# Optimization experiments

Measured on AMD Instinct MI355X. Metric: run time of the kernel, lower is better.

Reference implementation:

```python
import jax, jax.numpy as jnp
import numpy as np

E, H, D = 1024, 16, 64
F = 4608          # max_ffn_size = int(1024*3*1.5)
BASE_FFN = 3072   # int(emb*3)
ADAPT = 0.5
CHUNK = 256


def rotate_half(x):
    x1 = x[..., ::2]
    x2 = x[..., 1::2]
    return jnp.stack((-x2, x1), axis=-1).reshape(x.shape[:-1] + (-1,))


def rms_norm(x, w, eps=1e-6):
    x = jnp.where(jnp.isnan(x) | jnp.isinf(x), jnp.zeros_like(x), x)
    rms = jnp.clip(jnp.sqrt(jnp.mean(x * x, axis=-1, keepdims=True) + eps), 1e-6, 1e6)
    return x / rms * w


def setup_inputs() -> dict:
    key = jax.random.key(0)
    ks = jax.random.split(key, 12)
    s = 0.02
    return {
        "x": jax.random.normal(ks[0], (2, 4096, E), dtype=jnp.float32),
        "w_qkv": jax.random.normal(ks[1], (E, 3 * E), dtype=jnp.float32) * s,
        "w_out": jax.random.normal(ks[2], (E, E), dtype=jnp.float32) * s,
        "g1": jnp.ones((E,), dtype=jnp.float32),
        "g2": jnp.ones((E,), dtype=jnp.float32),
        "w_dp1": jax.random.normal(ks[3], (E, E // 4), dtype=jnp.float32) * s,
        "w_dp2": jax.random.normal(ks[4], (E // 4, 1), dtype=jnp.float32) * s,
        "w_gate": jax.random.normal(ks[5], (E, F), dtype=jnp.float32) * s,
        "w_up": jax.random.normal(ks[6], (E, F), dtype=jnp.float32) * s,
        "w_down": jax.random.normal(ks[7], (F, E), dtype=jnp.float32) * s,
        "g_hidden": jnp.ones((F,), dtype=jnp.float32),
    }


def _linear_attention(x, w_qkv, w_out):
    B, L, _ = x.shape
    qkv = (x @ w_qkv).reshape(B, L, 3, H, D).transpose(2, 0, 3, 1, 4)  # [3,B,H,L,D]
    q, k, v = qkv[0], qkv[1], qkv[2]
    # RoPE (start_pos = 0)
    pos = jnp.arange(L, dtype=jnp.float32)
    inv_freq = 1.0 / (10000.0 ** (jnp.arange(0, D, 2, dtype=jnp.float32) / D))
    freqs = pos[:, None] * inv_freq[None, :]
    emb = jnp.concatenate([freqs, freqs], axis=-1)
    cos = jnp.cos(emb)[None, None]
    sin = jnp.sin(emb)[None, None]
    q = q * cos + rotate_half(q) * sin
    k = k * cos + rotate_half(k) * sin
    # elu + 1 feature map
    q = jax.nn.elu(q) + 1.0
    k = jax.nn.elu(k) + 1.0
    # chunk-wise cumulative recurrence (no cache path)
    NC = L // CHUNK
    def to_chunks(t):
        return jnp.moveaxis(t.reshape(B, H, NC, CHUNK, D), 2, 0)  # [NC,B,H,C,D]
    qc, kc, vc = to_chunks(q), to_chunks(k), to_chunks(v)

    def step(carry, inp):
        S, Z = carry  # S:[B,H,D,D], Z:[B,H,D]
        qi, ki, vi = inp
        kv = jnp.einsum('bhld,bhle->bhlde', ki, vi)
        kv_cum = jnp.cumsum(kv, axis=2) + S[:, :, None]
        k_cum = jnp.cumsum(ki, axis=2) + Z[:, :, None]
        num = jnp.einsum('bhld,bhlde->bhle', qi, kv_cum)
        den = jnp.einsum('bhld,bhld->bhl', qi, k_cum)
        return (kv_cum[:, :, -1], k_cum[:, :, -1]), (num, den)

    S0 = jnp.zeros((B, H, D, D), dtype=x.dtype)
    Z0 = jnp.zeros((B, H, D), dtype=x.dtype)
    _, (num, den) = jax.lax.scan(step, (S0, Z0), (qc, kc, vc))
    num = jnp.moveaxis(num, 0, 2).reshape(B, H, L, D)
    den = jnp.moveaxis(den, 0, 2).reshape(B, H, L)
    den = jnp.maximum(den, 1e-6)
    out = num / den[..., None]
    out = out.transpose(0, 2, 1, 3).reshape(B, L, H * D)
    return out @ w_out


def _adaptive_ffn(x, w_dp1, w_dp2, w_gate, w_up, w_down, g_hidden):
    x_mean = x.mean(axis=1)                                   # [B,E]
    dim_ratio = jax.nn.sigmoid(jax.nn.silu(x_mean @ w_dp1) @ w_dp2)  # [B,1]
    ratio = jnp.clip(1.0 + (dim_ratio - 0.5) * 2.0 * ADAPT, 1.0 - ADAPT, 1.0 + ADAPT)
    size = jnp.maximum(1, jnp.floor(BASE_FFN * ratio.mean())).astype(jnp.int32)
    mask = (jnp.arange(F) < size).astype(x.dtype)             # [F]
    gate = jax.nn.silu(x @ w_gate) * mask
    up = (x @ w_up) * mask
    hidden = gate * up
    hidden = jnp.where(jnp.isnan(hidden) | jnp.isinf(hidden), jnp.zeros_like(hidden), hidden)
    # RMSNorm over the first `size` features only (matches sliced torch RMSNorm)
    rms = jnp.sqrt(jnp.sum(hidden * hidden, axis=-1, keepdims=True) / size.astype(x.dtype) + 1e-6)
    rms = jnp.clip(rms, 1e-6, 1e6)
    hidden = hidden / rms * g_hidden * mask                   # padded-to-F hidden
    return hidden @ w_down


def reference(x, w_qkv, w_out, g1, g2, w_dp1, w_dp2, w_gate, w_up, w_down, g_hidden):
    # pre-norm residual block: x + attn(norm1(x)); then x + ffn(norm2(x))
    h = rms_norm(x, g1)
    x = x + _linear_attention(h, w_qkv, w_out)
    h2 = rms_norm(x, g2)
    x = x + _adaptive_ffn(h2, w_dp1, w_dp2, w_gate, w_up, w_down, g_hidden)
    return x
```

## Files before the change

kernel.cpp:

```cpp
#include <hip/hip_runtime.h>
#include <hip/hip_bf16.h>

#define Ee 1024
#define Hh 16
#define Ff 4608
#define Ll 4096
#define Bb 2
#define NCc 16
#define CHk 256

typedef short bf16x8 __attribute__((ext_vector_type(8)));
typedef float f32x4 __attribute__((ext_vector_type(4)));

#define GLD16(g, l) __builtin_amdgcn_global_load_lds( \
    (const __attribute__((address_space(1))) unsigned int*)(g), \
    (__attribute__((address_space(3))) unsigned int*)(l), 16, 0, 0)

__device__ __forceinline__ unsigned short f2bf(float f){
  unsigned int u = __builtin_bit_cast(unsigned int, f);
  u += 0x7fffu + ((u >> 16) & 1u);
  return (unsigned short)(u >> 16);
}
__device__ __forceinline__ float bf2f(unsigned short h){
  unsigned int u = ((unsigned int)h) << 16;
  return __builtin_bit_cast(float, u);
}
__device__ __forceinline__ float fixv(float v){
  return (__builtin_isnan(v) || __builtin_isinf(v)) ? 0.f : v;
}

__global__ __launch_bounds__(256) void wconv_kernel(const float* __restrict__ W,
    unsigned short* __restrict__ WT, int K, int N, const float* __restrict__ scale){
  __shared__ unsigned short T[64][72];
  int k0 = blockIdx.y*64, n0 = blockIdx.x*64;
  int t = threadIdx.x;
  int kr = t>>4, n4 = (t&15)*4;
  #pragma unroll
  for (int it=0; it<4; it++){
    int k = kr + it*16;
    float s = scale ? scale[k0+k] : 1.f;
    float4 v = *(const float4*)(W + (size_t)(k0+k)*N + n0 + n4);
    T[n4+0][k] = f2bf(v.x*s);
    T[n4+1][k] = f2bf(v.y*s);
    T[n4+2][k] = f2bf(v.z*s);
    T[n4+3][k] = f2bf(v.w*s);
  }
  __syncthreads();
  int u = t&7;
  #pragma unroll
  for (int it=0; it<2; it++){
    int n = (t>>3) + it*32;
    *(bf16x8*)(WT + (size_t)(n0+n)*K + k0 + u*8) = *(const bf16x8*)&T[n][u*8];
  }
}

__global__ __launch_bounds__(256) void rmsnorm_kernel(const float* __restrict__ x,
    const float* __restrict__ g, unsigned short* __restrict__ out){
  int row = blockIdx.x; int t = threadIdx.x;
  float4 v = ((const float4*)(x + (size_t)row*Ee))[t];
  v.x=fixv(v.x); v.y=fixv(v.y); v.z=fixv(v.z); v.w=fixv(v.w);
  float ss = v.x*v.x + v.y*v.y + v.z*v.z + v.w*v.w;
  #pragma unroll
  for (int off=32; off>0; off>>=1) ss += __shfl_down(ss, off);
  __shared__ float red[4];
  if ((t&63)==0) red[t>>6] = ss;
  __syncthreads();
  float tot = red[0]+red[1]+red[2]+red[3];
  float rms = sqrtf(tot*(1.f/Ee) + 1e-6f);
  rms = fminf(fmaxf(rms, 1e-6f), 1e6f);
  float inv = 1.f/rms;
  float4 gv = ((const float4*)g)[t];
  uint2 o;
  o.x = (unsigned)f2bf(v.x*inv*gv.x) | ((unsigned)f2bf(v.y*inv*gv.y)<<16);
  o.y = (unsigned)f2bf(v.z*inv*gv.z) | ((unsigned)f2bf(v.w*inv*gv.w)<<16);
  ((uint2*)(out + (size_t)row*Ee))[t] = o;
}

template<int MODE>
__global__ __launch_bounds__(512) void gemm_kernel(
    const unsigned short* __restrict__ A, const unsigned short* __restrict__ Bt,
    void* __restrict__ Cv, int M, int N, int K,
    const float* __restrict__ res, const float* __restrict__ rowscale,
    const float* __restrict__ klim){
  __shared__ __align__(16) unsigned short S[2][12288];
  int tid = threadIdx.x;
  int nbx = gridDim.x;
  int id = blockIdx.y * nbx + blockIdx.x;
  int chunk = (nbx * gridDim.y) >> 3;
  int wg = (id & 7) * chunk + (id >> 3);
  int m0 = (wg / nbx) * 256, n0 = (wg % nbx) * 128;
  int lane = tid & 63, wave = tid >> 6;
  int wm = (wave>>1)*64, wn = (wave&1)*64;
  int lrow = lane & 15;
  int lksw = (((lane>>4) ^ ((lrow>>1)&3)))*8;
  int kend = K;
  if (MODE==2 && klim){
    int sz = (int)klim[0];
    int ke = ((sz + 31) >> 5) << 5;
    kend = ke < K ? ke : K;
  }
  int nk = kend >> 5;
  int segr = lane >> 2;
  int cg = (((lane&3) ^ ((lane>>3)&3))) * 8;
  const unsigned short* gp[3];
  int loff[3];
  #pragma unroll
  for (int i=0;i<3;i++){
    int g = wave*3 + i;
    if (g < 16){ gp[i] = A  + (size_t)(m0 + g*16 + segr)*K + cg;       loff[i] = g*512 + lane*8; }
    else       { gp[i] = Bt + (size_t)(n0 + (g-16)*16 + segr)*K + cg;  loff[i] = 8192 + (g-16)*512 + lane*8; }
  }
  f32x4 acc[4][4] = {};
  #pragma unroll
  for (int i=0;i<3;i++) GLD16(gp[i], &S[0][loff[i] - lane*8]);
  __syncthreads();
  int cur = 0;
  for (int t=0; t<nk; ++t){
    if (t+1 < nk){
      int ko = (t+1) << 5;
      #pragma unroll
      for (int i=0;i<3;i++) GLD16(gp[i]+ko, &S[cur^1][loff[i] - lane*8]);
    }
    bf16x8 af[4], bfr[4];
    #pragma unroll
    for (int i=0;i<4;i++){
      af[i]  = *(const bf16x8*)&S[cur][(wm + i*16 + lrow)*32 + lksw];
      bfr[i] = *(const bf16x8*)&S[cur][8192 + (wn + i*16 + lrow)*32 + lksw];
    }
    #pragma unroll
    for (int mi=0;mi<4;mi++)
      #pragma unroll
      for (int ni=0;ni<4;ni++)
        acc[mi][ni] = __builtin_amdgcn_mfma_f32_16x16x32_bf16(af[mi], bfr[ni], acc[mi][ni], 0,0,0);
    __syncthreads();
    cur ^= 1;
  }
  int lg = lane >> 4;
  int rbase = m0 + wm + (lg<<2);
  int cbase = n0 + wn + lrow;
  #pragma unroll
  for (int mi=0;mi<4;mi++){
    #pragma unroll
    for (int r=0;r<4;r++){
      int row = rbase + mi*16 + r;
      float rs = (MODE==2) ? rowscale[row] : 1.f;
      #pragma unroll
      for (int ni=0;ni<4;ni++){
        int col = cbase + ni*16;
        float v = acc[mi][ni][r];
        if (MODE==0){
          ((unsigned short*)Cv)[(size_t)row*N + col] = f2bf(v);
        } else if (MODE==1){
          ((float*)Cv)[(size_t)row*N + col] = v + res[(size_t)row*N + col];
        } else {
          ((float*)Cv)[(size_t)row*N + col] = v*rs + res[(size_t)row*N + col];
        }
      }
    }
  }
}

__global__ __launch_bounds__(512) void gateup_kernel(
    const unsigned short* __restrict__ A, const unsigned short* __restrict__ Gt,
    const unsigned short* __restrict__ Ut, unsigned short* __restrict__ Hid,
    const float* __restrict__ scal){
  __shared__ __align__(16) unsigned short S[2][16384];
  int tid = threadIdx.x;
  int nbx = gridDim.x;
  int id = blockIdx.y * nbx + blockIdx.x;
  int chunk = (nbx * gridDim.y) >> 3;
  int wg = (id & 7) * chunk + (id >> 3);
  int m0 = (wg / nbx) * 256, n0 = (wg % nbx) * 128;
  int size = (int)scal[0];
  if (n0 >= size){
    int r = tid >> 1, cb = n0 + (tid&1)*64;
    unsigned short* hp = Hid + (size_t)(m0+r)*Ff + cb;
    bf16x8 z = {};
    #pragma unroll
    for (int i=0;i<8;i++) *(bf16x8*)(hp + i*8) = z;
    return;
  }
  int lane = tid & 63, wave = tid >> 6;
  int wm = (wave>>1)*64, wn = (wave&1)*64;
  int lrow = lane & 15;
  int lksw = (((lane>>4) ^ ((lrow>>1)&3)))*8;
  int segr = lane >> 2;
  int cg = (((lane&3) ^ ((lane>>3)&3))) * 8;
  const unsigned short* gp[4];
  int loff[4];
  #pragma unroll
  for (int i=0;i<4;i++){
    int g = wave*4 + i;
    if (g < 16)      { gp[i] = A  + (size_t)(m0 + g*16 + segr)*Ee + cg;       loff[i] = g*512; }
    else if (g < 24) { gp[i] = Gt + (size_t)(n0 + (g-16)*16 + segr)*Ee + cg;  loff[i] = 8192 + (g-16)*512; }
    else             { gp[i] = Ut + (size_t)(n0 + (g-24)*16 + segr)*Ee + cg;  loff[i] = 12288 + (g-24)*512; }
  }
  f32x4 ag[4][4] = {}, au[4][4] = {};
  #pragma unroll
  for (int i=0;i<4;i++) GLD16(gp[i], &S[0][loff[i]]);
  __syncthreads();
  int cur = 0;
  for (int t=0; t<32; ++t){
    if (t+1 < 32){
      int ko = (t+1) << 5;
      #pragma unroll
      for (int i=0;i<4;i++) GLD16(gp[i]+ko, &S[cur^1][loff[i]]);
    }
    bf16x8 af[4], bg4[4], bu4[4];
    #pragma unroll
    for (int i=0;i<4;i++){
      af[i]  = *(const bf16x8*)&S[cur][(wm + i*16 + lrow)*32 + lksw];
      bg4[i] = *(const bf16x8*)&S[cur][8192  + (wn + i*16 + lrow)*32 + lksw];
      bu4[i] = *(const bf16x8*)&S[cur][12288 + (wn + i*16 + lrow)*32 + lksw];
    }
    #pragma unroll
    for (int mi=0;mi<4;mi++)
      #pragma unroll
      for (int ni=0;ni<4;ni++){
        ag[mi][ni] = __builtin_amdgcn_mfma_f32_16x16x32_bf16(af[mi], bg4[ni], ag[mi][ni], 0,0,0);
        au[mi][ni] = __builtin_amdgcn_mfma_f32_16x16x32_bf16(af[mi], bu4[ni], au[mi][ni], 0,0,0);
      }
    __syncthreads();
    cur ^= 1;
  }
  int lg = lane >> 4;
  int rbase = m0 + wm + (lg<<2);
  int cbase = n0 + wn + lrow;
  #pragma unroll
  for (int mi=0;mi<4;mi++){
    #pragma unroll
    for (int r=0;r<4;r++){
      int row = rbase + mi*16 + r;
      #pragma unroll
      for (int ni=0;ni<4;ni++){
        int col = cbase + ni*16;
        float g = ag[mi][ni][r], u = au[mi][ni][r];
        float hv = (g * (1.f/(1.f+expf(-g)))) * u;
        if (col >= size) hv = 0.f;
        if (__builtin_isnan(hv) || __builtin_isinf(hv)) hv = 0.f;
        Hid[(size_t)row*Ff + col] = f2bf(hv);
      }
    }
  }
}

__global__ __launch_bounds__(256) void rope_kernel(unsigned short* __restrict__ qkv){
  size_t idx = (size_t)blockIdx.x*256 + threadIdx.x;
  int i = (int)(idx & 31);
  int h = (int)((idx>>5) & 15);
  size_t bl = idx >> 9;
  int pos = (int)(bl & (Ll-1));
  int d0 = 2*i, d1 = d0+1;
  size_t base = bl*3072 + (size_t)h*64 + d0;
  const float LOG1E4_D32 = 0.2878231366242557f;
  float e0 = (float)(d0 < 32 ? d0 : d0-32);
  float e1 = (float)(d1 < 32 ? d1 : d1-32);
  float f0 = pos * expf(-e0*LOG1E4_D32);
  float f1 = pos * expf(-e1*LOG1E4_D32);
  float s0,c0,s1,c1;
  sincosf(f0,&s0,&c0); sincosf(f1,&s1,&c1);
  unsigned int* qp = (unsigned int*)(qkv + base);
  unsigned int qv = *qp;
  float q0 = bf2f((unsigned short)(qv&0xffff)), q1 = bf2f((unsigned short)(qv>>16));
  float r0 = q0*c0 - q1*s0;
  float r1 = q1*c1 + q0*s1;
  r0 = r0>0.f ? r0+1.f : expf(r0);
  r1 = r1>0.f ? r1+1.f : expf(r1);
  *qp = (unsigned)f2bf(r0) | ((unsigned)f2bf(r1)<<16);
  unsigned int* kp = (unsigned int*)(qkv + base + 1024);
  unsigned int kv = *kp;
  float k0v = bf2f((unsigned short)(kv&0xffff)), k1v = bf2f((unsigned short)(kv>>16));
  float t0 = k0v*c0 - k1v*s0;
  float t1 = k1v*c1 + k0v*s1;
  t0 = t0>0.f ? t0+1.f : expf(t0);
  t1 = t1>0.f ? t1+1.f : expf(t1);
  *kp = (unsigned)f2bf(t0) | ((unsigned)f2bf(t1)<<16);
}

__global__ __launch_bounds__(256) void chunksum_kernel(const unsigned short* __restrict__ qkv,
    float* __restrict__ Ssum){
  __shared__ __align__(16) unsigned short Kt[64][72];
  __shared__ __align__(16) unsigned short Vt[80][72];
  int c = blockIdx.x, bh = blockIdx.y;
  int b = bh >> 4, h = bh & 15;
  int tid = threadIdx.x, lane = tid & 63, wave = tid >> 6;
  int lr = lane & 15, lg = lane >> 4;
  f32x4 acc[5] = {};
  {
    int r16 = tid >> 4, m4 = (tid & 15) * 4;
    unsigned short val = (r16 == 0) ? (unsigned short)0x3F80 : (unsigned short)0;
    #pragma unroll
    for (int u=0; u<4; u++) Vt[64 + r16][m4 + u] = val;
  }
  for (int t=0; t<4; ++t){
    __syncthreads();
    #pragma unroll
    for (int i=0; i<2; i++){
      int tau = tid + i*256;
      int m = tau & 63, dg = (tau >> 6) * 8;
      size_t g = ((size_t)(b*Ll + c*CHk + t*64 + m))*3072 + h*64 + dg;
      bf16x8 kv = *(const bf16x8*)(qkv + g + 1024);
      bf16x8 vv = *(const bf16x8*)(qkv + g + 2048);
      #pragma unroll
      for (int u=0; u<8; u++){
        Kt[dg+u][m] = (unsigned short)kv[u];
        Vt[dg+u][m] = (unsigned short)vv[u];
      }
    }
    __syncthreads();
    #pragma unroll
    for (int kk=0; kk<2; kk++){
      bf16x8 af = *(const bf16x8*)&Kt[wave*16 + lr][kk*32 + lg*8];
      #pragma unroll
      for (int ni=0; ni<5; ni++){
        bf16x8 vf = *(const bf16x8*)&Vt[ni*16 + lr][kk*32 + lg*8];
        acc[ni] = __builtin_amdgcn_mfma_f32_16x16x32_bf16(af, vf, acc[ni], 0,0,0);
      }
    }
  }
  float* S = Ssum + ((size_t)bh*NCc + c)*4160;
  int j = wave*16 + lg*4;
  #pragma unroll
  for (int ni=0; ni<4; ni++)
    #pragma unroll
    for (int r=0; r<4; r++)
      S[(size_t)(j+r)*64 + ni*16 + lr] = acc[ni][r];
  if (lr == 0){
    #pragma unroll
    for (int r=0; r<4; r++) S[4096 + j + r] = acc[4][r];
  }
}

__global__ __launch_bounds__(256) void prefix_kernel(const float* __restrict__ Ssum,
    float* __restrict__ Spre){
  int bh = blockIdx.x; int t = threadIdx.x;
  size_t base = (size_t)bh*NCc*4160;
  for (int e=t; e<4160; e+=256){
    float acc = 0.f;
    #pragma unroll
    for (int c=0;c<NCc;c++){
      Spre[base + (size_t)c*4160 + e] = acc;
      acc += Ssum[base + (size_t)c*4160 + e];
    }
  }
}

__global__ __launch_bounds__(256, 2) void attnout_kernel(const unsigned short* __restrict__ qkv,
    const float* __restrict__ Spre, unsigned short* __restrict__ attn){
  __shared__ __align__(16) unsigned short SpT[64][72];
  __shared__ __align__(16) unsigned short Ks[64][72];
  __shared__ __align__(16) unsigned short Vt[64][72];
  __shared__ __align__(16) unsigned short P[4][64][72];
  __shared__ float qZd[256];
  int c = blockIdx.x, bh = blockIdx.y;
  int b = bh >> 4, h = bh & 15;
  int tid = threadIdx.x, lane = tid & 63, wave = tid >> 6;
  int lr = lane & 15, lg = lane >> 4;
  const float* Sp = Spre + ((size_t)bh*NCc + c)*4160;

  {
    float zacc = 0.f;
    const unsigned short* qp = qkv + ((size_t)(b*Ll + c*CHk + tid))*3072 + (size_t)h*64;
    #pragma unroll
    for (int g8=0; g8<8; g8++){
      bf16x8 qv = *(const bf16x8*)(qp + g8*8);
      #pragma unroll
      for (int u=0; u<8; u++) zacc += bf2f((unsigned short)qv[u]) * Sp[4096 + g8*8 + u];
    }
    qZd[tid] = zacc;
  }
  #pragma unroll
  for (int i=0; i<2; i++){
    int tau = tid + i*256;
    int j = tau & 63, dg = (tau >> 6) * 8;
    const float* sp = Sp + j*64 + dg;
    #pragma unroll
    for (int u=0; u<8; u++) SpT[dg+u][j] = f2bf(sp[u]);
  }
  bf16x8 af[4][2];
  #pragma unroll
  for (int mi=0; mi<4; mi++){
    size_t qrow = ((size_t)(b*Ll + c*CHk + wave*64 + mi*16 + lr))*3072 + (size_t)h*64;
    #pragma unroll
    for (int kk=0; kk<2; kk++)
      af[mi][kk] = *(const bf16x8*)(qkv + qrow + kk*32 + lg*8);
  }
  __syncthreads();
  f32x4 accO[4][4] = {};
  #pragma unroll
  for (int kk=0; kk<2; kk++){
    #pragma unroll
    for (int ni=0; ni<4; ni++){
      bf16x8 bsp = *(const bf16x8*)&SpT[ni*16 + lr][kk*32 + lg*8];
      #pragma unroll
      for (int mi=0; mi<4; mi++)
        accO[mi][ni] = __builtin_amdgcn_mfma_f32_16x16x32_bf16(af[mi][kk], bsp, accO[mi][ni], 0,0,0);
    }
  }
  f32x4 den4[4] = {};
  for (int t=0; t<4; ++t){
    __syncthreads();
    #pragma unroll
    for (int i=0; i<2; i++){
      int tau = tid + i*256;
      int m = tau & 63, dg = (tau >> 6) * 8;
      size_t g = ((size_t)(b*Ll + c*CHk + t*64 + m))*3072 + h*64 + dg;
      *(bf16x8*)&Ks[m][dg] = *(const bf16x8*)(qkv + g + 1024);
      bf16x8 vv = *(const bf16x8*)(qkv + g + 2048);
      #pragma unroll
      for (int u=0; u<8; u++) Vt[dg+u][m] = (unsigned short)vv[u];
    }
    __syncthreads();
    if (wave < t) continue;
    f32x4 sacc[4][4] = {};
    #pragma unroll
    for (int kk=0; kk<2; kk++){
      #pragma unroll
      for (int ni=0; ni<4; ni++){
        bf16x8 kf = *(const bf16x8*)&Ks[ni*16 + lr][kk*32 + lg*8];
        #pragma unroll
        for (int mi=0; mi<4; mi++)
          sacc[mi][ni] = __builtin_amdgcn_mfma_f32_16x16x32_bf16(af[mi][kk], kf, sacc[mi][ni], 0,0,0);
      }
    }
    unsigned short (*Pw)[72] = P[wave];
    bool diag = (t == wave);
    #pragma unroll
    for (int mi=0; mi<4; mi++){
      #pragma unroll
      for (int r=0; r<4; r++){
        int q_l = mi*16 + lg*4 + r;
        float rs = 0.f;
        #pragma unroll
        for (int ni=0; ni<4; ni++){
          int m_l = ni*16 + lr;
          float v = sacc[mi][ni][r];
          if (diag && m_l > q_l) v = 0.f;
          rs += v;
          Pw[q_l][m_l] = f2bf(v);
        }
        rs += __shfl_xor(rs, 1);
        rs += __shfl_xor(rs, 2);
        rs += __shfl_xor(rs, 4);
        rs += __shfl_xor(rs, 8);
        den4[mi][r] += rs;
      }
    }
    #pragma unroll
    for (int kk=0; kk<2; kk++){
      bf16x8 pa[4], vf[4];
      #pragma unroll
      for (int mi=0; mi<4; mi++) pa[mi] = *(const bf16x8*)&Pw[mi*16 + lr][kk*32 + lg*8];
      #pragma unroll
      for (int ni=0; ni<4; ni++) vf[ni] = *(const bf16x8*)&Vt[ni*16 + lr][kk*32 + lg*8];
      #pragma unroll
      for (int mi=0; mi<4; mi++)
        #pragma unroll
        for (int ni=0; ni<4; ni++)
          accO[mi][ni] = __builtin_amdgcn_mfma_f32_16x16x32_bf16(pa[mi], vf[ni], accO[mi][ni], 0,0,0);
    }
  }
  #pragma unroll
  for (int mi=0; mi<4; mi++){
    #pragma unroll
    for (int r=0; r<4; r++){
      int q_l = mi*16 + lg*4 + r;
      float dtot = den4[mi][r] + qZd[wave*64 + q_l];
      float inv = 1.f / fmaxf(dtot, 1e-6f);
      size_t l = (size_t)(b*Ll + c*CHk + wave*64 + q_l);
      unsigned short* op = attn + l*Ee + h*64 + lr;
      #pragma unroll
      for (int ni=0; ni<4; ni++)
        op[ni*16] = f2bf(accO[mi][ni][r] * inv);
    }
  }
}

__global__ __launch_bounds__(256) void colmean1_kernel(const unsigned short* __restrict__ h2,
    float* __restrict__ partial){
  int e = blockIdx.x*256 + threadIdx.x;
  int ly = blockIdx.y;
  int b = blockIdx.z;
  int l0 = ly * 128;
  float s = 0.f;
  for (int l=l0; l<l0+128; l++) s += bf2f(h2[((size_t)(b*Ll + l))*Ee + e]);
  partial[((size_t)(b*32 + ly))*Ee + e] = s;
}
__global__ __launch_bounds__(256) void colmean2_kernel(const float* __restrict__ partial,
    float* __restrict__ xmean){
  int e = blockIdx.x*256 + threadIdx.x;
  int b = blockIdx.y;
  float s = 0.f;
  #pragma unroll
  for (int ly=0; ly<32; ly++) s += partial[((size_t)(b*32 + ly))*Ee + e];
  xmean[b*Ee + e] = s * (1.f/Ll);
}

__global__ __launch_bounds__(256) void dimpred_kernel(const float* __restrict__ xmean,
    const float* __restrict__ w_dp1, const float* __restrict__ w_dp2,
    float* __restrict__ scalars){
  __shared__ float red[256];
  __shared__ float ratio_s[2];
  int t = threadIdx.x;
  for (int b=0;b<2;b++){
    float s = 0.f;
    for (int k=0;k<1024;k++) s += xmean[b*Ee + k] * w_dp1[k*256 + t];
    float sil = s * (1.f/(1.f+expf(-s)));
    red[t] = sil * w_dp2[t];
    __syncthreads();
    for (int off=128; off>0; off>>=1){
      if (t<off) red[t] += red[t+off];
      __syncthreads();
    }
    if (t==0){
      float dr = 1.f/(1.f+expf(-red[0]));
      float ratio = 1.f + (dr-0.5f)*1.0f;
      ratio = fminf(fmaxf(ratio, 0.5f), 1.5f);
      ratio_s[b] = ratio;
    }
    __syncthreads();
  }
  if (t==0){
    float rm = 0.5f*(ratio_s[0]+ratio_s[1]);
    float size_f = floorf(3072.f * rm);
    if (size_f < 1.f) size_f = 1.f;
    scalars[0] = size_f;
  }
}

__global__ __launch_bounds__(256) void rowrms_kernel(const unsigned short* __restrict__ Hid,
    const float* __restrict__ scal, float* __restrict__ invr){
  int row = blockIdx.x; int t = threadIdx.x;
  float size_f = scal[0];
  int c8max = ((int)size_f + 7) >> 3;
  float ss = 0.f;
  for (int c8 = t; c8 < c8max; c8 += 256){
    bf16x8 v = *(const bf16x8*)(Hid + (size_t)row*Ff + c8*8);
    #pragma unroll
    for (int u=0;u<8;u++){ float f = bf2f((unsigned short)v[u]); ss += f*f; }
  }
  #pragma unroll
  for (int off=32; off>0; off>>=1) ss += __shfl_down(ss, off);
  __shared__ float red[4];
  if ((t&63)==0) red[t>>6] = ss;
  __syncthreads();
  if (t==0){
    float tot = red[0]+red[1]+red[2]+red[3];
    float rms = sqrtf(tot/size_f + 1e-6f);
    rms = fminf(fmaxf(rms, 1e-6f), 1e6f);
    invr[row] = 1.f/rms;
  }
}

extern "C" void kernel_launch(void* const* d_in, const int* in_sizes, int n_in,
                              void* d_out, int out_size, void* d_ws, size_t ws_size,
                              hipStream_t stream){
  const float* x      = (const float*)d_in[0];
  const float* w_qkv  = (const float*)d_in[1];
  const float* w_out  = (const float*)d_in[2];
  const float* g1     = (const float*)d_in[3];
  const float* g2     = (const float*)d_in[4];
  const float* w_dp1  = (const float*)d_in[5];
  const float* w_dp2  = (const float*)d_in[6];
  const float* w_gate = (const float*)d_in[7];
  const float* w_up   = (const float*)d_in[8];
  const float* w_down = (const float*)d_in[9];
  const float* g_hid  = (const float*)d_in[10];
  float* out = (float*)d_out;

  char* w = (char*)d_ws;
  size_t o = 0;
  auto alloc = [&](size_t bytes)->char*{ char* p = w + o; o += (bytes + 255) & ~255ull; return p; };
  unsigned short* R1   = (unsigned short*)alloc((size_t)8192*1024*2);
  float*          x2   = (float*)alloc((size_t)8192*1024*4);
  char*           R2   = alloc((size_t)8192*4608*2);
  unsigned short* qkvT = (unsigned short*)alloc((size_t)3072*1024*2);
  unsigned short* outT = (unsigned short*)alloc((size_t)1024*1024*2);
  char*           W2   = alloc((size_t)3*4608*1024*2);
  float*       partial = (float*)alloc((size_t)64*1024*4);
  float*         xmean = (float*)alloc(2048*4);
  float*          scal = (float*)alloc(64);
  float*          invr = (float*)alloc(8192*4);

  unsigned short* qkv    = (unsigned short*)R2;
  unsigned short* hidden = (unsigned short*)R2;
  float* Ssum = (float*)W2;
  float* Spre = Ssum + (size_t)512*4160;
  unsigned short* gateT = (unsigned short*)W2;
  unsigned short* upT   = gateT + (size_t)4608*1024;
  unsigned short* downT = upT   + (size_t)4608*1024;

  wconv_kernel<<<dim3(3072/64, 1024/64),256,0,stream>>>(w_qkv, qkvT, 1024, 3072, nullptr);
  wconv_kernel<<<dim3(1024/64, 1024/64),256,0,stream>>>(w_out, outT, 1024, 1024, nullptr);

  rmsnorm_kernel<<<8192,256,0,stream>>>(x, g1, R1);
  gemm_kernel<0><<<dim3(3072/128, 8192/256),512,0,stream>>>(R1, qkvT, qkv,
      8192,3072,1024, nullptr,nullptr,nullptr);
  rope_kernel<<<16384,256,0,stream>>>(qkv);
  chunksum_kernel<<<dim3(NCc,Bb*Hh),256,0,stream>>>(qkv, Ssum);
  prefix_kernel<<<Bb*Hh,256,0,stream>>>(Ssum, Spre);
  attnout_kernel<<<dim3(NCc,Bb*Hh),256,0,stream>>>(qkv, Spre, R1);

  wconv_kernel<<<dim3(4608/64, 1024/64),256,0,stream>>>(w_gate, gateT, 1024, 4608, nullptr);
  wconv_kernel<<<dim3(4608/64, 1024/64),256,0,stream>>>(w_up,   upT,   1024, 4608, nullptr);
  wconv_kernel<<<dim3(1024/64, 4608/64),256,0,stream>>>(w_down, downT, 4608, 1024, g_hid);

  gemm_kernel<1><<<dim3(1024/128, 8192/256),512,0,stream>>>(R1, outT, x2,
      8192,1024,1024, x,nullptr,nullptr);
  rmsnorm_kernel<<<8192,256,0,stream>>>(x2, g2, R1);
  colmean1_kernel<<<dim3(4,32,2),256,0,stream>>>(R1, partial);
  colmean2_kernel<<<dim3(4,2),256,0,stream>>>(partial, xmean);
  dimpred_kernel<<<1,256,0,stream>>>(xmean, w_dp1, w_dp2, scal);
  gateup_kernel<<<dim3(4608/128, 8192/256),512,0,stream>>>(R1, gateT, upT, hidden, scal);
  rowrms_kernel<<<8192,256,0,stream>>>(hidden, scal, invr);
  gemm_kernel<2><<<dim3(1024/128, 8192/256),512,0,stream>>>(hidden, downT, out,
      8192,1024,4608, x2, invr, scal);
}
```

Measured before the change: 514.9 us.

## Fuse hidden row sum-of-squares into gateup epilogue and double GEMM k-tile

Computes per-row sum of squares of the FFN hidden directly in the gate/up epilogue via shuffles and atomicAdd, removing the separate rowrms pass that re-read the full hidden matrix. The down GEMM now derives the inverse RMS from the sum itself. Both GEMM kernels also process a 64-wide k step per pipeline stage with an intra-stage barrier and raised wave priority around MFMAs, halving loop/barrier count. This doubles LDS use, which may reduce occupancy, and adds atomics and a memset.

```diff
diff --git a/kernel.cpp b/kernel.cpp
--- a/kernel.cpp
+++ b/kernel.cpp
@@ -82,7 +82,7 @@
     void* __restrict__ Cv, int M, int N, int K,
     const float* __restrict__ res, const float* __restrict__ rowscale,
     const float* __restrict__ klim){
-  __shared__ __align__(16) unsigned short S[2][12288];
+  __shared__ __align__(16) unsigned short S[2][24576];
   int tid = threadIdx.x;
   int nbx = gridDim.x;
   int id = blockIdx.y * nbx + blockIdx.x;
@@ -93,13 +93,14 @@
   int wm = (wave>>1)*64, wn = (wave&1)*64;
   int lrow = lane & 15;
   int lksw = (((lane>>4) ^ ((lrow>>1)&3)))*8;
+  float klim0 = (MODE==2 && klim) ? klim[0] : 0.f;
   int kend = K;
   if (MODE==2 && klim){
-    int sz = (int)klim[0];
-    int ke = ((sz + 31) >> 5) << 5;
+    int sz = (int)klim0;
+    int ke = ((sz + 63) >> 6) << 6;
     kend = ke < K ? ke : K;
   }
-  int nk = kend >> 5;
+  int nk2 = kend >> 6;
   int segr = lane >> 2;
   int cg = (((lane&3) ^ ((lane>>3)&3))) * 8;
   const unsigned short* gp[3];
@@ -107,31 +108,44 @@
   #pragma unroll
   for (int i=0;i<3;i++){
     int g = wave*3 + i;
-    if (g < 16){ gp[i] = A  + (size_t)(m0 + g*16 + segr)*K + cg;       loff[i] = g*512 + lane*8; }
-    else       { gp[i] = Bt + (size_t)(n0 + (g-16)*16 + segr)*K + cg;  loff[i] = 8192 + (g-16)*512 + lane*8; }
+    if (g < 16){ gp[i] = A  + (size_t)(m0 + g*16 + segr)*K + cg;       loff[i] = g*512; }
+    else       { gp[i] = Bt + (size_t)(n0 + (g-16)*16 + segr)*K + cg;  loff[i] = 8192 + (g-16)*512; }
   }
   f32x4 acc[4][4] = {};
   #pragma unroll
-  for (int i=0;i<3;i++) GLD16(gp[i], &S[0][loff[i] - lane*8]);
+  for (int i=0;i<3;i++){
+    GLD16(gp[i],    &S[0][loff[i]]);
+    GLD16(gp[i]+32, &S[0][12288 + loff[i]]);
+  }
   __syncthreads();
   int cur = 0;
-  for (int t=0; t<nk; ++t){
-    if (t+1 < nk){
-      int ko = (t+1) << 5;
-      #pragma unroll
-      for (int i=0;i<3;i++) GLD16(gp[i]+ko, &S[cur^1][loff[i] - lane*8]);
-    }
-    bf16x8 af[4], bfr[4];
-    #pragma unroll
-    for (int i=0;i<4;i++){
-      af[i]  = *(const bf16x8*)&S[cur][(wm + i*16 + lrow)*32 + lksw];
-      bfr[i] = *(const bf16x8*)&S[cur][8192 + (wn + i*16 + lrow)*32 + lksw];
-    }
-    #pragma unroll
-    for (int mi=0;mi<4;mi++)
-      #pragma unroll
-      for (int ni=0;ni<4;ni++)
-        acc[mi][ni] = __builtin_amdgcn_mfma_f32_16x16x32_bf16(af[mi], bfr[ni], acc[mi][ni], 0,0,0);
+  for (int t=0; t<nk2; ++t){
+    if (t+1 < nk2){
+      int ko = (t+1) << 6;
+      #pragma unroll
+      for (int i=0;i<3;i++){
+        GLD16(gp[i]+ko,    &S[cur^1][loff[i]]);
+        GLD16(gp[i]+ko+32, &S[cur^1][12288 + loff[i]]);
+      }
+    }
+    #pragma unroll
+    for (int kk=0; kk<2; kk++){
+      int base = kk*12288;
+      bf16x8 af[4], bfr[4];
+      #pragma unroll
+      for (int i=0;i<4;i++){
+        af[i]  = *(const bf16x8*)&S[cur][base + (wm + i*16 + lrow)*32 + lksw];
+        bfr[i] = *(const bf16x8*)&S[cur][base + 8192 + (wn + i*16 + lrow)*32 + lksw];
+      }
+      __builtin_amdgcn_s_setprio(1);
+      #pragma unroll
+      for (int mi=0;mi<4;mi++)
+        #pragma unroll
+        for (int ni=0;ni<4;ni++)
+          acc[mi][ni] = __builtin_amdgcn_mfma_f32_16x16x32_bf16(af[mi], bfr[ni], acc[mi][ni], 0,0,0);
+      __builtin_amdgcn_s_setprio(0);
+      if (kk==0) __builtin_amdgcn_s_barrier();
+    }
     __syncthreads();
     cur ^= 1;
   }
@@ -143,7 +157,12 @@
     #pragma unroll
     for (int r=0;r<4;r++){
       int row = rbase + mi*16 + r;
-      float rs = (MODE==2) ? rowscale[row] : 1.f;
+      float rs = 1.f;
+      if (MODE==2){
+        float rms = sqrtf(rowscale[row]/klim0 + 1e-6f);
+        rms = fminf(fmaxf(rms, 1e-6f), 1e6f);
+        rs = 1.f/rms;
+      }
       #pragma unroll
       for (int ni=0;ni<4;ni++){
         int col = cbase + ni*16;
@@ -163,8 +182,8 @@
 __global__ __launch_bounds__(512) void gateup_kernel(
     const unsigned short* __restrict__ A, const unsigned short* __restrict__ Gt,
     const unsigned short* __restrict__ Ut, unsigned short* __restrict__ Hid,
-    const float* __restrict__ scal){
-  __shared__ __align__(16) unsigned short S[2][16384];
+    const float* __restrict__ scal, float* __restrict__ sumsq){
+  __shared__ __align__(16) unsigned short S[2][32768];
   int tid = threadIdx.x;
   int nbx = gridDim.x;
   int id = blockIdx.y * nbx + blockIdx.x;
@@ -197,40 +216,55 @@
   }
   f32x4 ag[4][4] = {}, au[4][4] = {};
   #pragma unroll
-  for (int i=0;i<4;i++) GLD16(gp[i], &S[0][loff[i]]);
+  for (int i=0;i<4;i++){
+    GLD16(gp[i],    &S[0][loff[i]]);
+    GLD16(gp[i]+32, &S[0][16384 + loff[i]]);
+  }
   __syncthreads();
   int cur = 0;
-  for (int t=0; t<32; ++t){
-    if (t+1 < 32){
-      int ko = (t+1) << 5;
-      #pragma unroll
-      for (int i=0;i<4;i++) GLD16(gp[i]+ko, &S[cur^1][loff[i]]);
-    }
-    bf16x8 af[4], bg4[4], bu4[4];
-    #pragma unroll
-    for (int i=0;i<4;i++){
-      af[i]  = *(const bf16x8*)&S[cur][(wm + i*16 + lrow)*32 + lksw];
-      bg4[i] = *(const bf16x8*)&S[cur][8192  + (wn + i*16 + lrow)*32 + lksw];
-      bu4[i] = *(const bf16x8*)&S[cur][12288 + (wn + i*16 + lrow)*32 + lksw];
-    }
-    #pragma unroll
-    for (int mi=0;mi<4;mi++)
-      #pragma unroll
-      for (int ni=0;ni<4;ni++){
-        ag[mi][ni] = __builtin_amdgcn_mfma_f32_16x16x32_bf16(af[mi], bg4[ni], ag[mi][ni], 0,0,0);
-        au[mi][ni] = __builtin_amdgcn_mfma_f32_16x16x32_bf16(af[mi], bu4[ni], au[mi][ni], 0,0,0);
-      }
+  for (int t=0; t<16; ++t){
+    if (t+1 < 16){
+      int ko = (t+1) << 6;
+      #pragma unroll
+      for (int i=0;i<4;i++){
+        GLD16(gp[i]+ko,    &S[cur^1][loff[i]]);
+        GLD16(gp[i]+ko+32, &S[cur^1][16384 + loff[i]]);
+      }
+    }
+    #pragma unroll
+    for (int kk=0; kk<2; kk++){
+      int base = kk*16384;
+      bf16x8 af[4], bg4[4], bu4[4];
+      #pragma unroll
+      for (int i=0;i<4;i++){
+        af[i]  = *(const bf16x8*)&S[cur][base + (wm + i*16 + lrow)*32 + lksw];
+        bg4[i] = *(const bf16x8*)&S[cur][base + 8192  + (wn + i*16 + lrow)*32 + lksw];
+        bu4[i] = *(const bf16x8*)&S[cur][base + 12288 + (wn + i*16 + lrow)*32 + lksw];
+      }
+      __builtin_amdgcn_s_setprio(1);
+      #pragma unroll
+      for (int mi=0;mi<4;mi++)
+        #pragma unroll
+        for (int ni=0;ni<4;ni++){
+          ag[mi][ni] = __builtin_amdgcn_mfma_f32_16x16x32_bf16(af[mi], bg4[ni], ag[mi][ni], 0,0,0);
+          au[mi][ni] = __builtin_amdgcn_mfma_f32_16x16x32_bf16(af[mi], bu4[ni], au[mi][ni], 0,0,0);
+        }
+      __builtin_amdgcn_s_setprio(0);
+      if (kk==0) __builtin_amdgcn_s_barrier();
+    }
     __syncthreads();
     cur ^= 1;
   }
   int lg = lane >> 4;
+  int lr = lrow;
   int rbase = m0 + wm + (lg<<2);
-  int cbase = n0 + wn + lrow;
+  int cbase = n0 + wn + lr;
   #pragma unroll
   for (int mi=0;mi<4;mi++){
     #pragma unroll
     for (int r=0;r<4;r++){
       int row = rbase + mi*16 + r;
+      float s4 = 0.f;
       #pragma unroll
       for (int ni=0;ni<4;ni++){
         int col = cbase + ni*16;
@@ -239,7 +273,13 @@
         if (col >= size) hv = 0.f;
         if (__builtin_isnan(hv) || __builtin_isinf(hv)) hv = 0.f;
         Hid[(size_t)row*Ff + col] = f2bf(hv);
-      }
+        s4 += hv*hv;
+      }
+      s4 += __shfl_xor(s4, 1);
+      s4 += __shfl_xor(s4, 2);
+      s4 += __shfl_xor(s4, 4);
+      s4 += __shfl_xor(s4, 8);
+      if (lr == 0) atomicAdd(&sumsq[row], s4);
     }
   }
 }
@@ -528,30 +568,6 @@
   }
 }
 
-__global__ __launch_bounds__(256) void rowrms_kernel(const unsigned short* __restrict__ Hid,
-    const float* __restrict__ scal, float* __restrict__ invr){
-  int row = blockIdx.x; int t = threadIdx.x;
-  float size_f = scal[0];
-  int c8max = ((int)size_f + 7) >> 3;
-  float ss = 0.f;
-  for (int c8 = t; c8 < c8max; c8 += 256){
-    bf16x8 v = *(const bf16x8*)(Hid + (size_t)row*Ff + c8*8);
-    #pragma unroll
-    for (int u=0;u<8;u++){ float f = bf2f((unsigned short)v[u]); ss += f*f; }
-  }
-  #pragma unroll
-  for (int off=32; off>0; off>>=1) ss += __shfl_down(ss, off);
-  __shared__ float red[4];
-  if ((t&63)==0) red[t>>6] = ss;
-  __syncthreads();
-  if (t==0){
-    float tot = red[0]+red[1]+red[2]+red[3];
-    float rms = sqrtf(tot/size_f + 1e-6f);
-    rms = fminf(fmaxf(rms, 1e-6f), 1e6f);
-    invr[row] = 1.f/rms;
-  }
-}
-
 extern "C" void kernel_launch(void* const* d_in, const int* in_sizes, int n_in,
                               void* d_out, int out_size, void* d_ws, size_t ws_size,
                               hipStream_t stream){
@@ -580,7 +596,7 @@
   float*       partial = (float*)alloc((size_t)64*1024*4);
   float*         xmean = (float*)alloc(2048*4);
   float*          scal = (float*)alloc(64);
-  float*          invr = (float*)alloc(8192*4);
+  float*         sumsq = (float*)alloc(8192*4);
 
   unsigned short* qkv    = (unsigned short*)R2;
   unsigned short* hidden = (unsigned short*)R2;
@@ -611,8 +627,8 @@
   colmean1_kernel<<<dim3(4,32,2),256,0,stream>>>(R1, partial);
   colmean2_kernel<<<dim3(4,2),256,0,stream>>>(partial, xmean);
   dimpred_kernel<<<1,256,0,stream>>>(xmean, w_dp1, w_dp2, scal);
-  gateup_kernel<<<dim3(4608/128, 8192/256),512,0,stream>>>(R1, gateT, upT, hidden, scal);
-  rowrms_kernel<<<8192,256,0,stream>>>(hidden, scal, invr);
+  hipMemsetAsync(sumsq, 0, 8192*sizeof(float), stream);
+  gateup_kernel<<<dim3(4608/128, 8192/256),512,0,stream>>>(R1, gateT, upT, hidden, scal, sumsq);
   gemm_kernel<2><<<dim3(1024/128, 8192/256),512,0,stream>>>(hidden, downT, out,
-      8192,1024,4608, x2, invr, scal);
-}
+      8192,1024,4608, x2, sumsq, scal);
+}
```

Result: faster. 489.3 us (-5.0%).
